# Kernel optimization log

Hardware: AMD Instinct MI355X
Metric: run time of the kernel (lower is better)

Reference implementation:

```python
import jax, jax.numpy as jnp
import numpy as np

D_MODEL = 1024
N_HEAD = 16
D_K = D_MODEL // N_HEAD
B, T = 4, 2048


def setup_inputs() -> dict:
    key = jax.random.key(0)
    ks = jax.random.split(key, 12)
    s = 1.0 / np.sqrt(D_MODEL)
    inp = {
        "q": jax.random.normal(ks[0], (B, T, D_MODEL), jnp.float32),
        "k": jax.random.normal(ks[1], (B, T, D_MODEL), jnp.float32),
        "v": jax.random.normal(ks[2], (B, T, D_MODEL), jnp.float32),
        # causal mask: True = allowed
        "mask": jnp.tril(jnp.ones((T, T), bool))[None, None, :, :],
        "w_q": jax.random.uniform(ks[3], (D_MODEL, D_MODEL), jnp.float32, -s, s),
        "b_q": jax.random.uniform(ks[4], (D_MODEL,), jnp.float32, -s, s),
        "w_k": jax.random.uniform(ks[5], (D_MODEL, D_MODEL), jnp.float32, -s, s),
        "b_k": jax.random.uniform(ks[6], (D_MODEL,), jnp.float32, -s, s),
        "w_v": jax.random.uniform(ks[7], (D_MODEL, D_MODEL), jnp.float32, -s, s),
        "b_v": jax.random.uniform(ks[8], (D_MODEL,), jnp.float32, -s, s),
        "w_o": jax.random.uniform(ks[9], (D_MODEL, D_MODEL), jnp.float32, -s, s),
        "b_o": jax.random.uniform(ks[10], (D_MODEL,), jnp.float32, -s, s),
    }
    return inp


def reference(q, k, v, mask, w_q, b_q, w_k, b_k, w_v, b_v, w_o, b_o):
    b, tq, d = q.shape
    tk = k.shape[1]
    # projections (torch Linear: x @ W^T + b)
    qh = (q @ w_q.T + b_q).reshape(b, tq, N_HEAD, D_K).transpose(0, 2, 1, 3)
    kh = (k @ w_k.T + b_k).reshape(b, tk, N_HEAD, D_K).transpose(0, 2, 1, 3)
    vh = (v @ w_v.T + b_v).reshape(b, tk, N_HEAD, D_K).transpose(0, 2, 1, 3)
    # scores: (b, h, tq, tk)
    scores = jnp.einsum("bhqd,bhkd->bhqk", qh, kh) / jnp.sqrt(jnp.float32(D_K))
    scores = jnp.where(mask, scores, jnp.finfo(scores.dtype).min)
    attn = jax.nn.softmax(scores, axis=-1)
    out = jnp.einsum("bhqk,bhkd->bhqd", attn, vh)
    out = out.transpose(0, 2, 1, 3).reshape(b, tq, d)
    return out @ w_o.T + b_o
```

## Files before the change

kernel.cpp:

```cpp
#include <hip/hip_runtime.h>

typedef unsigned short u16;
typedef __attribute__((ext_vector_type(8))) short bf16x8;
typedef __attribute__((ext_vector_type(4))) float f32x4;

#define D_MODEL 1024
#define T_SEQ   2048
#define NB      4
#define NH      16
#define DKH     64

__device__ __forceinline__ u16 f2bf(float x) {
  union { float f; unsigned u; } v; v.f = x;
  unsigned r = v.u + 0x7fffu + ((v.u >> 16) & 1u);
  return (u16)(r >> 16);
}
__device__ __forceinline__ unsigned pack2(float a, float b) {
  return (unsigned)f2bf(a) | ((unsigned)f2bf(b) << 16);
}

__device__ __forceinline__ void gload16(const void* g, void* l) {
  __builtin_amdgcn_global_load_lds(
      (const __attribute__((address_space(1))) unsigned*)g,
      (__attribute__((address_space(3))) unsigned*)l, 16, 0, 0);
}

__global__ void cast_w4(const float* __restrict__ s0, const float* __restrict__ s1,
                        const float* __restrict__ s2, const float* __restrict__ s3,
                        u16* __restrict__ o0, u16* __restrict__ o1,
                        u16* __restrict__ o2, u16* __restrict__ o3) {
  const int which = blockIdx.y;
  const float* s = which == 0 ? s0 : which == 1 ? s1 : which == 2 ? s2 : s3;
  u16* o = which == 0 ? o0 : which == 1 ? o1 : which == 2 ? o2 : o3;
  int i = ((int)blockIdx.x * 256 + (int)threadIdx.x) * 4;
  float4 v = *(const float4*)(s + i);
  uint2 u; u.x = pack2(v.x, v.y); u.y = pack2(v.z, v.w);
  *(uint2*)(o + i) = u;
}

__global__ void cast_x1(const float* __restrict__ s, u16* __restrict__ o) {
  size_t i = ((size_t)blockIdx.x * 256 + threadIdx.x) * 4;
  float4 v = *(const float4*)(s + i);
  uint2 u; u.x = pack2(v.x, v.y); u.y = pack2(v.z, v.w);
  *(uint2*)(o + i) = u;
}

template<int OUT_BF16>
__global__ __launch_bounds__(256) void gemm_nt(const u16* __restrict__ Ab,
                                               const u16* __restrict__ W,
                                               const float* __restrict__ bias,
                                               void* __restrict__ Cp,
                                               int M, int N, int K) {
  __shared__ __align__(16) u16 As[128 * 64];
  __shared__ __align__(16) u16 Bs[128 * 64];
  const int tid = threadIdx.x;
  const int w = tid >> 6, lane = tid & 63;
  const int wm = w & 1, wn = w >> 1;
  const int l15 = lane & 15, quad = lane >> 4;
  const int m0 = blockIdx.x * 128, n0 = blockIdx.y * 128;
  const int lrow = lane >> 3;
  const int lcol = ((lane & 7) ^ lrow) * 8;

  const u16* gA = Ab + (size_t)(m0 + w * 32 + lrow) * K + lcol;
  const u16* gB = W  + (size_t)(n0 + w * 32 + lrow) * K + lcol;
  u16* lA = As + w * 32 * 64;
  u16* lB = Bs + w * 32 * 64;

  f32x4 zero4 = {0.f, 0.f, 0.f, 0.f};
  f32x4 acc[4][4];
#pragma unroll
  for (int i = 0; i < 4; ++i)
#pragma unroll
    for (int j = 0; j < 4; ++j) acc[i][j] = zero4;

  for (int kb = 0; kb < K; kb += 64) {
    __syncthreads();
#pragma unroll
    for (int t = 0; t < 4; ++t) gload16(gA + kb + t * 8 * K, lA + t * 512);
#pragma unroll
    for (int t = 0; t < 4; ++t) gload16(gB + kb + t * 8 * K, lB + t * 512);
    __syncthreads();

#pragma unroll
    for (int ks = 0; ks < 2; ++ks) {
      const int sA = (((ks * 4 + quad) ^ (l15 & 7)) * 8);
      bf16x8 af[4], bfr[4];
#pragma unroll
      for (int i = 0; i < 4; ++i)
        af[i] = *(const bf16x8*)(As + (wm * 64 + i * 16 + l15) * 64 + sA);
#pragma unroll
      for (int i = 0; i < 4; ++i)
        bfr[i] = *(const bf16x8*)(Bs + (wn * 64 + i * 16 + l15) * 64 + sA);
#pragma unroll
      for (int mi = 0; mi < 4; ++mi)
#pragma unroll
        for (int ni = 0; ni < 4; ++ni)
          acc[mi][ni] = __builtin_amdgcn_mfma_f32_16x16x32_bf16(af[mi], bfr[ni], acc[mi][ni], 0, 0, 0);
    }
  }

#pragma unroll
  for (int ni = 0; ni < 4; ++ni) {
    int col = n0 + wn * 64 + ni * 16 + l15;
    float bv = bias[col];
#pragma unroll
    for (int mi = 0; mi < 4; ++mi) {
      int row = m0 + wm * 64 + mi * 16 + quad * 4;
#pragma unroll
      for (int r = 0; r < 4; ++r) {
        float vv = acc[mi][ni][r] + bv;
        if (OUT_BF16) ((u16*)Cp)[(size_t)(row + r) * N + col] = f2bf(vv);
        else          ((float*)Cp)[(size_t)(row + r) * N + col] = vv;
      }
    }
  }
}

__global__ __launch_bounds__(256) void attn_fwd(const u16* __restrict__ Xq,
                                                const u16* __restrict__ Xk,
                                                const u16* __restrict__ Xv,
                                                u16* __restrict__ O) {
  __shared__ __align__(16) u16 Vt[2][64 * 72];

  const int xp = blockIdx.x;
  const int h = blockIdx.y, b = blockIdx.z;
  const int tid = threadIdx.x;
  const int w = tid >> 6, lane = tid & 63;
  const int l15 = lane & 15, quad = lane >> 4;
  const size_t base = (size_t)b * T_SEQ * D_MODEL;
  const int hd = h * DKH;
  const int vkey = tid & 63, vdp = tid >> 6;
  const int skey = (vkey & 0x20) | ((vkey & 0xC) << 1) | ((vkey & 0x10) >> 2) | (vkey & 3);

  bf16x8 bones;
#pragma unroll
  for (int i = 0; i < 8; ++i) bones[i] = (short)0x3F80;

  f32x4 zero4 = {0.f, 0.f, 0.f, 0.f};
  int tcnt = 0;

  for (int ph = 0; ph < 2; ++ph) {
    const int qt = ph ? xp : 15 - xp;
    const int q0 = qt * 128;
    const int rowb0 = q0 + w * 32;

    bf16x8 bq[2][2];
#pragma unroll
    for (int mi = 0; mi < 2; ++mi)
#pragma unroll
      for (int ks = 0; ks < 2; ++ks)
        bq[mi][ks] = *(const bf16x8*)(Xq + base + (size_t)(rowb0 + mi * 16 + l15) * D_MODEL
                                      + hd + ks * 32 + quad * 8);

    f32x4 o[4][2], ol[2];
#pragma unroll
    for (int di = 0; di < 4; ++di)
#pragma unroll
      for (int mi = 0; mi < 2; ++mi) o[di][mi] = zero4;
#pragma unroll
    for (int mi = 0; mi < 2; ++mi) ol[mi] = zero4;
    float m_s[2] = {-1e30f, -1e30f};

    const int nkt = 2 * qt + 2;
    for (int kt = 0; kt < nkt; ++kt, ++tcnt) {
      const int k0 = kt * 64;
      const int buf = tcnt & 1;

      const u16* vp = Xv + base + (size_t)(k0 + vkey) * D_MODEL + hd + vdp * 16;
      uint4 va0 = *(const uint4*)vp;
      uint4 va1 = *(const uint4*)(vp + 8);

      bf16x8 ak[4][2];
#pragma unroll
      for (int ni = 0; ni < 4; ++ni) {
        const u16* kp = Xk + base + (size_t)(k0 + ni * 16 + l15) * D_MODEL + hd + quad * 8;
        ak[ni][0] = *(const bf16x8*)kp;
        ak[ni][1] = *(const bf16x8*)(kp + 32);
      }

      {
        union { uint4 u; u16 hh[8]; } u0, u1;
        u0.u = va0; u1.u = va1;
        u16* vtb = Vt[buf];
#pragma unroll
        for (int i = 0; i < 8; ++i) {
          vtb[(vdp * 16 + i) * 72 + skey] = u0.hh[i];
          vtb[(vdp * 16 + 8 + i) * 72 + skey] = u1.hh[i];
        }
      }

      f32x4 st[4][2];
#pragma unroll
      for (int ni = 0; ni < 4; ++ni)
#pragma unroll
        for (int mi = 0; mi < 2; ++mi) {
          f32x4 t = zero4;
          t = __builtin_amdgcn_mfma_f32_16x16x32_bf16(ak[ni][0], bq[mi][0], t, 0, 0, 0);
          t = __builtin_amdgcn_mfma_f32_16x16x32_bf16(ak[ni][1], bq[mi][1], t, 0, 0, 0);
          st[ni][mi] = t;
        }

      bf16x8 bp[2][2];
#pragma unroll
      for (int mi = 0; mi < 2; ++mi) {
        const int qa = rowb0 + mi * 16 + l15;
        if (k0 + 63 > rowb0 + mi * 16) {
#pragma unroll
          for (int ni = 0; ni < 4; ++ni)
#pragma unroll
            for (int r = 0; r < 4; ++r)
              if (k0 + ni * 16 + quad * 4 + r > qa) st[ni][mi][r] = -1e30f;
        }
        float mx = st[0][mi][0];
#pragma unroll
        for (int ni = 0; ni < 4; ++ni)
#pragma unroll
          for (int r = 0; r < 4; ++r) mx = fmaxf(mx, st[ni][mi][r]);
        mx = fmaxf(mx, __shfl_xor(mx, 16));
        mx = fmaxf(mx, __shfl_xor(mx, 32));
        float mnew = fmaxf(m_s[mi], mx * 0.125f);
        float a = __expf(m_s[mi] - mnew);
        m_s[mi] = mnew;
#pragma unroll
        for (int r = 0; r < 4; ++r) ol[mi][r] *= a;
#pragma unroll
        for (int di = 0; di < 4; ++di)
#pragma unroll
          for (int r = 0; r < 4; ++r) o[di][mi][r] *= a;

        float p[4][4];
#pragma unroll
        for (int ni = 0; ni < 4; ++ni)
#pragma unroll
          for (int r = 0; r < 4; ++r)
            p[ni][r] = __expf(st[ni][mi][r] * 0.125f - mnew);
#pragma unroll
        for (int js = 0; js < 2; ++js) {
          union { bf16x8 v; unsigned d[4]; } ub;
          ub.d[0] = pack2(p[2 * js][0], p[2 * js][1]);
          ub.d[1] = pack2(p[2 * js][2], p[2 * js][3]);
          ub.d[2] = pack2(p[2 * js + 1][0], p[2 * js + 1][1]);
          ub.d[3] = pack2(p[2 * js + 1][2], p[2 * js + 1][3]);
          bp[mi][js] = ub.v;
        }
      }

      __syncthreads();

#pragma unroll
      for (int js = 0; js < 2; ++js) {
        bf16x8 av[4];
#pragma unroll
        for (int di = 0; di < 4; ++di)
          av[di] = *(const bf16x8*)(Vt[buf] + (di * 16 + l15) * 72 + js * 32 + quad * 8);
#pragma unroll
        for (int di = 0; di < 4; ++di)
#pragma unroll
          for (int mi = 0; mi < 2; ++mi)
            o[di][mi] = __builtin_amdgcn_mfma_f32_16x16x32_bf16(av[di], bp[mi][js], o[di][mi], 0, 0, 0);
#pragma unroll
        for (int mi = 0; mi < 2; ++mi)
          ol[mi] = __builtin_amdgcn_mfma_f32_16x16x32_bf16(bones, bp[mi][js], ol[mi], 0, 0, 0);
      }
    }

#pragma unroll
    for (int mi = 0; mi < 2; ++mi) {
      float inv = 1.0f / ol[mi][0];
      const size_t qa = rowb0 + mi * 16 + l15;
#pragma unroll
      for (int di = 0; di < 4; ++di) {
        uint2 s2;
        s2.x = pack2(o[di][mi][0] * inv, o[di][mi][1] * inv);
        s2.y = pack2(o[di][mi][2] * inv, o[di][mi][3] * inv);
        *(uint2*)(O + base + qa * D_MODEL + hd + di * 16 + quad * 4) = s2;
      }
    }
  }
}

extern "C" void kernel_launch(void* const* d_in, const int* in_sizes, int n_in,
                              void* d_out, int out_size, void* d_ws, size_t ws_size,
                              hipStream_t stream) {
  const float* q   = (const float*)d_in[0];
  const float* k   = (const float*)d_in[1];
  const float* v   = (const float*)d_in[2];
  const float* w_q = (const float*)d_in[4];  const float* b_q = (const float*)d_in[5];
  const float* w_k = (const float*)d_in[6];  const float* b_k = (const float*)d_in[7];
  const float* w_v = (const float*)d_in[8];  const float* b_v = (const float*)d_in[9];
  const float* w_o = (const float*)d_in[10]; const float* b_o = (const float*)d_in[11];

  u16* ws = (u16*)d_ws;
  const size_t NTD = (size_t)NB * T_SEQ * D_MODEL;
  const size_t WSZ = (size_t)D_MODEL * D_MODEL;
  u16* wqb = ws;
  u16* wkb = wqb + WSZ;
  u16* wvb = wkb + WSZ;
  u16* wob = wvb + WSZ;
  u16* Xq  = wob + WSZ;
  u16* Xk  = Xq + NTD;
  u16* Xv  = Xk + NTD;
  u16* Cb  = Xv + NTD;

  cast_w4<<<dim3(WSZ / 1024, 4), 256, 0, stream>>>(w_q, w_k, w_v, w_o, wqb, wkb, wvb, wob);

  dim3 g(64, 8, 1);
  cast_x1<<<NTD / 1024, 256, 0, stream>>>(q, Cb);
  gemm_nt<1><<<g, 256, 0, stream>>>(Cb, wqb, b_q, Xq, 8192, 1024, 1024);
  cast_x1<<<NTD / 1024, 256, 0, stream>>>(k, Cb);
  gemm_nt<1><<<g, 256, 0, stream>>>(Cb, wkb, b_k, Xk, 8192, 1024, 1024);
  cast_x1<<<NTD / 1024, 256, 0, stream>>>(v, Cb);
  gemm_nt<1><<<g, 256, 0, stream>>>(Cb, wvb, b_v, Xv, 8192, 1024, 1024);

  attn_fwd<<<dim3(8, NH, NB), 256, 0, stream>>>(Xq, Xk, Xv, Cb);

  gemm_nt<0><<<g, 256, 0, stream>>>(Cb, wob, b_o, d_out, 8192, 1024, 1024);
}
```

Before: 371.1 us.

## Fuse input cast into batched QKV GEMM and retile attention with prefetch

Replaces the separate fp32-to-bf16 cast kernels and three projection GEMMs with one batched QKV GEMM that reads fp32 activations and converts them in registers before storing to padded LDS. This drops the intermediate bf16 activation round-trip and several launches. The attention kernel moves from 128-row to 64-row query tiles with twice as many blocks, register-prefetches the next K/V tile, and uses exp2 with a folded scale. The cost is more register pressure from the prefetch and A loads that no longer use async global-to-LDS copies.

```diff
diff --git a/kernel.cpp b/kernel.cpp
--- a/kernel.cpp
+++ b/kernel.cpp
@@ -17,6 +17,13 @@
 }
 __device__ __forceinline__ unsigned pack2(float a, float b) {
   return (unsigned)f2bf(a) | ((unsigned)f2bf(b) << 16);
+}
+__device__ __forceinline__ float fexp2(float x) {
+#if __has_builtin(__builtin_amdgcn_exp2f)
+  return __builtin_amdgcn_exp2f(x);
+#else
+  return __expf(x * 0.6931471805599453f);
+#endif
 }
 
 __device__ __forceinline__ void gload16(const void* g, void* l) {
@@ -38,19 +45,95 @@
   *(uint2*)(o + i) = u;
 }
 
-__global__ void cast_x1(const float* __restrict__ s, u16* __restrict__ o) {
-  size_t i = ((size_t)blockIdx.x * 256 + threadIdx.x) * 4;
-  float4 v = *(const float4*)(s + i);
-  uint2 u; u.x = pack2(v.x, v.y); u.y = pack2(v.z, v.w);
-  *(uint2*)(o + i) = u;
-}
-
-template<int OUT_BF16>
-__global__ __launch_bounds__(256) void gemm_nt(const u16* __restrict__ Ab,
-                                               const u16* __restrict__ W,
-                                               const float* __restrict__ bias,
-                                               void* __restrict__ Cp,
-                                               int M, int N, int K) {
+__global__ __launch_bounds__(256) void gemm_qkv(
+    const float* __restrict__ qin, const float* __restrict__ kin, const float* __restrict__ vin,
+    const u16* __restrict__ wq, const u16* __restrict__ wk, const u16* __restrict__ wv,
+    const float* __restrict__ bqp, const float* __restrict__ bkp, const float* __restrict__ bvp,
+    u16* __restrict__ Xq, u16* __restrict__ Xk, u16* __restrict__ Xv) {
+  const int z = blockIdx.z;
+  const float* A = z == 0 ? qin : z == 1 ? kin : vin;
+  const u16* W = z == 0 ? wq : z == 1 ? wk : wv;
+  const float* bias = z == 0 ? bqp : z == 1 ? bkp : bvp;
+  u16* C = z == 0 ? Xq : z == 1 ? Xk : Xv;
+  const int K = 1024, N = 1024;
+
+  __shared__ __align__(16) u16 As[128 * 72];
+  __shared__ __align__(16) u16 Bs[128 * 64];
+  const int tid = threadIdx.x;
+  const int w = tid >> 6, lane = tid & 63;
+  const int wm = w & 1, wn = w >> 1;
+  const int l15 = lane & 15, quad = lane >> 4;
+  const int m0 = blockIdx.x * 128, n0 = blockIdx.y * 128;
+  const int srow = tid >> 3;
+  const int scol = (tid & 7) * 8;
+  const int lrow = lane >> 3;
+  const int lcol = ((lane & 7) ^ lrow) * 8;
+
+  const u16* gB = W + (size_t)(n0 + w * 32 + lrow) * K + lcol;
+  u16* lB = Bs + w * 32 * 64;
+
+  f32x4 zero4 = {0.f, 0.f, 0.f, 0.f};
+  f32x4 acc[4][4];
+#pragma unroll
+  for (int i = 0; i < 4; ++i)
+#pragma unroll
+    for (int j = 0; j < 4; ++j) acc[i][j] = zero4;
+
+  for (int kb = 0; kb < K; kb += 64) {
+    uint4 ra[4];
+#pragma unroll
+    for (int r = 0; r < 4; ++r) {
+      const float* p = A + (size_t)(m0 + r * 32 + srow) * K + kb + scol;
+      float4 x = *(const float4*)p;
+      float4 y = *(const float4*)(p + 4);
+      ra[r].x = pack2(x.x, x.y); ra[r].y = pack2(x.z, x.w);
+      ra[r].z = pack2(y.x, y.y); ra[r].w = pack2(y.z, y.w);
+    }
+    __syncthreads();
+#pragma unroll
+    for (int t = 0; t < 4; ++t) gload16(gB + kb + t * 8 * K, lB + t * 512);
+#pragma unroll
+    for (int r = 0; r < 4; ++r)
+      *(uint4*)(As + (r * 32 + srow) * 72 + scol) = ra[r];
+    __syncthreads();
+
+#pragma unroll
+    for (int ks = 0; ks < 2; ++ks) {
+      const int sB = (((ks * 4 + quad) ^ (l15 & 7)) * 8);
+      bf16x8 af[4], bfr[4];
+#pragma unroll
+      for (int i = 0; i < 4; ++i)
+        af[i] = *(const bf16x8*)(As + (wm * 64 + i * 16 + l15) * 72 + ks * 32 + quad * 8);
+#pragma unroll
+      for (int i = 0; i < 4; ++i)
+        bfr[i] = *(const bf16x8*)(Bs + (wn * 64 + i * 16 + l15) * 64 + sB);
+#pragma unroll
+      for (int mi = 0; mi < 4; ++mi)
+#pragma unroll
+        for (int ni = 0; ni < 4; ++ni)
+          acc[mi][ni] = __builtin_amdgcn_mfma_f32_16x16x32_bf16(af[mi], bfr[ni], acc[mi][ni], 0, 0, 0);
+    }
+  }
+
+#pragma unroll
+  for (int ni = 0; ni < 4; ++ni) {
+    int col = n0 + wn * 64 + ni * 16 + l15;
+    float bv = bias[col];
+#pragma unroll
+    for (int mi = 0; mi < 4; ++mi) {
+      int row = m0 + wm * 64 + mi * 16 + quad * 4;
+#pragma unroll
+      for (int r = 0; r < 4; ++r)
+        C[(size_t)(row + r) * N + col] = f2bf(acc[mi][ni][r] + bv);
+    }
+  }
+}
+
+__global__ __launch_bounds__(256) void gemm_nt_f32out(const u16* __restrict__ Ab,
+                                                      const u16* __restrict__ W,
+                                                      const float* __restrict__ bias,
+                                                      float* __restrict__ Cp,
+                                                      int M, int N, int K) {
   __shared__ __align__(16) u16 As[128 * 64];
   __shared__ __align__(16) u16 Bs[128 * 64];
   const int tid = threadIdx.x;
@@ -107,11 +190,8 @@
     for (int mi = 0; mi < 4; ++mi) {
       int row = m0 + wm * 64 + mi * 16 + quad * 4;
 #pragma unroll
-      for (int r = 0; r < 4; ++r) {
-        float vv = acc[mi][ni][r] + bv;
-        if (OUT_BF16) ((u16*)Cp)[(size_t)(row + r) * N + col] = f2bf(vv);
-        else          ((float*)Cp)[(size_t)(row + r) * N + col] = vv;
-      }
+      for (int r = 0; r < 4; ++r)
+        Cp[(size_t)(row + r) * N + col] = acc[mi][ni][r] + bv;
     }
   }
 }
@@ -136,47 +216,47 @@
 #pragma unroll
   for (int i = 0; i < 8; ++i) bones[i] = (short)0x3F80;
 
+  const float cs = 0.18033688f;
   f32x4 zero4 = {0.f, 0.f, 0.f, 0.f};
   int tcnt = 0;
 
   for (int ph = 0; ph < 2; ++ph) {
-    const int qt = ph ? xp : 15 - xp;
-    const int q0 = qt * 128;
-    const int rowb0 = q0 + w * 32;
-
-    bf16x8 bq[2][2];
-#pragma unroll
-    for (int mi = 0; mi < 2; ++mi)
-#pragma unroll
-      for (int ks = 0; ks < 2; ++ks)
-        bq[mi][ks] = *(const bf16x8*)(Xq + base + (size_t)(rowb0 + mi * 16 + l15) * D_MODEL
-                                      + hd + ks * 32 + quad * 8);
-
-    f32x4 o[4][2], ol[2];
-#pragma unroll
-    for (int di = 0; di < 4; ++di)
-#pragma unroll
-      for (int mi = 0; mi < 2; ++mi) o[di][mi] = zero4;
-#pragma unroll
-    for (int mi = 0; mi < 2; ++mi) ol[mi] = zero4;
-    float m_s[2] = {-1e30f, -1e30f};
-
-    const int nkt = 2 * qt + 2;
+    const int qt = ph ? xp : 31 - xp;
+    const int q0 = qt * 64;
+    const int rowb = q0 + w * 16;
+    const int qa = rowb + l15;
+
+    bf16x8 bq[2];
+#pragma unroll
+    for (int ks = 0; ks < 2; ++ks)
+      bq[ks] = *(const bf16x8*)(Xq + base + (size_t)(rowb + l15) * D_MODEL
+                                + hd + ks * 32 + quad * 8);
+
+    f32x4 o[4], ol;
+#pragma unroll
+    for (int di = 0; di < 4; ++di) o[di] = zero4;
+    ol = zero4;
+    float m2 = -1e30f;
+
+    const int nkt = qt + 1;
+
+    uint4 va0, va1;
+    bf16x8 ak[4][2];
+    {
+      const u16* vp = Xv + base + (size_t)vkey * D_MODEL + hd + vdp * 16;
+      va0 = *(const uint4*)vp;
+      va1 = *(const uint4*)(vp + 8);
+#pragma unroll
+      for (int ni = 0; ni < 4; ++ni) {
+        const u16* kp = Xk + base + (size_t)(ni * 16 + l15) * D_MODEL + hd + quad * 8;
+        ak[ni][0] = *(const bf16x8*)kp;
+        ak[ni][1] = *(const bf16x8*)(kp + 32);
+      }
+    }
+
     for (int kt = 0; kt < nkt; ++kt, ++tcnt) {
       const int k0 = kt * 64;
       const int buf = tcnt & 1;
-
-      const u16* vp = Xv + base + (size_t)(k0 + vkey) * D_MODEL + hd + vdp * 16;
-      uint4 va0 = *(const uint4*)vp;
-      uint4 va1 = *(const uint4*)(vp + 8);
-
-      bf16x8 ak[4][2];
-#pragma unroll
-      for (int ni = 0; ni < 4; ++ni) {
-        const u16* kp = Xk + base + (size_t)(k0 + ni * 16 + l15) * D_MODEL + hd + quad * 8;
-        ak[ni][0] = *(const bf16x8*)kp;
-        ak[ni][1] = *(const bf16x8*)(kp + 32);
-      }
 
       {
         union { uint4 u; u16 hh[8]; } u0, u1;
@@ -189,60 +269,71 @@
         }
       }
 
-      f32x4 st[4][2];
+      const bool pf = (kt + 1 < nkt);
+      uint4 nva0, nva1;
+      bf16x8 nak[4][2];
+      if (pf) {
+        const int nk0 = k0 + 64;
+        const u16* vp = Xv + base + (size_t)(nk0 + vkey) * D_MODEL + hd + vdp * 16;
+        nva0 = *(const uint4*)vp;
+        nva1 = *(const uint4*)(vp + 8);
+#pragma unroll
+        for (int ni = 0; ni < 4; ++ni) {
+          const u16* kp = Xk + base + (size_t)(nk0 + ni * 16 + l15) * D_MODEL + hd + quad * 8;
+          nak[ni][0] = *(const bf16x8*)kp;
+          nak[ni][1] = *(const bf16x8*)(kp + 32);
+        }
+      }
+
+      f32x4 st[4];
+#pragma unroll
+      for (int ni = 0; ni < 4; ++ni) {
+        f32x4 t = zero4;
+        t = __builtin_amdgcn_mfma_f32_16x16x32_bf16(ak[ni][0], bq[0], t, 0, 0, 0);
+        t = __builtin_amdgcn_mfma_f32_16x16x32_bf16(ak[ni][1], bq[1], t, 0, 0, 0);
+        st[ni] = t;
+      }
+
+      if (k0 + 63 > rowb) {
+#pragma unroll
+        for (int ni = 0; ni < 4; ++ni)
+#pragma unroll
+          for (int r = 0; r < 4; ++r)
+            if (k0 + ni * 16 + quad * 4 + r > qa) st[ni][r] = -1e30f;
+      }
+
+      float mx = st[0][0];
 #pragma unroll
       for (int ni = 0; ni < 4; ++ni)
 #pragma unroll
-        for (int mi = 0; mi < 2; ++mi) {
-          f32x4 t = zero4;
-          t = __builtin_amdgcn_mfma_f32_16x16x32_bf16(ak[ni][0], bq[mi][0], t, 0, 0, 0);
-          t = __builtin_amdgcn_mfma_f32_16x16x32_bf16(ak[ni][1], bq[mi][1], t, 0, 0, 0);
-          st[ni][mi] = t;
-        }
-
-      bf16x8 bp[2][2];
-#pragma unroll
-      for (int mi = 0; mi < 2; ++mi) {
-        const int qa = rowb0 + mi * 16 + l15;
-        if (k0 + 63 > rowb0 + mi * 16) {
-#pragma unroll
-          for (int ni = 0; ni < 4; ++ni)
-#pragma unroll
-            for (int r = 0; r < 4; ++r)
-              if (k0 + ni * 16 + quad * 4 + r > qa) st[ni][mi][r] = -1e30f;
-        }
-        float mx = st[0][mi][0];
-#pragma unroll
-        for (int ni = 0; ni < 4; ++ni)
-#pragma unroll
-          for (int r = 0; r < 4; ++r) mx = fmaxf(mx, st[ni][mi][r]);
-        mx = fmaxf(mx, __shfl_xor(mx, 16));
-        mx = fmaxf(mx, __shfl_xor(mx, 32));
-        float mnew = fmaxf(m_s[mi], mx * 0.125f);
-        float a = __expf(m_s[mi] - mnew);
-        m_s[mi] = mnew;
-#pragma unroll
-        for (int r = 0; r < 4; ++r) ol[mi][r] *= a;
-#pragma unroll
-        for (int di = 0; di < 4; ++di)
-#pragma unroll
-          for (int r = 0; r < 4; ++r) o[di][mi][r] *= a;
-
-        float p[4][4];
-#pragma unroll
-        for (int ni = 0; ni < 4; ++ni)
-#pragma unroll
-          for (int r = 0; r < 4; ++r)
-            p[ni][r] = __expf(st[ni][mi][r] * 0.125f - mnew);
-#pragma unroll
-        for (int js = 0; js < 2; ++js) {
-          union { bf16x8 v; unsigned d[4]; } ub;
-          ub.d[0] = pack2(p[2 * js][0], p[2 * js][1]);
-          ub.d[1] = pack2(p[2 * js][2], p[2 * js][3]);
-          ub.d[2] = pack2(p[2 * js + 1][0], p[2 * js + 1][1]);
-          ub.d[3] = pack2(p[2 * js + 1][2], p[2 * js + 1][3]);
-          bp[mi][js] = ub.v;
-        }
+        for (int r = 0; r < 4; ++r) mx = fmaxf(mx, st[ni][r]);
+      mx = fmaxf(mx, __shfl_xor(mx, 16));
+      mx = fmaxf(mx, __shfl_xor(mx, 32));
+      const float m2new = fmaxf(m2, mx * cs);
+      const float a = fexp2(m2 - m2new);
+      m2 = m2new;
+      ol[0] *= a;
+#pragma unroll
+      for (int di = 0; di < 4; ++di)
+#pragma unroll
+        for (int r = 0; r < 4; ++r) o[di][r] *= a;
+
+      float p[4][4];
+#pragma unroll
+      for (int ni = 0; ni < 4; ++ni)
+#pragma unroll
+        for (int r = 0; r < 4; ++r)
+          p[ni][r] = fexp2(fmaf(st[ni][r], cs, -m2new));
+
+      bf16x8 bp[2];
+#pragma unroll
+      for (int js = 0; js < 2; ++js) {
+        union { bf16x8 v; unsigned d[4]; } ub;
+        ub.d[0] = pack2(p[2 * js][0], p[2 * js][1]);
+        ub.d[1] = pack2(p[2 * js][2], p[2 * js][3]);
+        ub.d[2] = pack2(p[2 * js + 1][0], p[2 * js + 1][1]);
+        ub.d[3] = pack2(p[2 * js + 1][2], p[2 * js + 1][3]);
+        bp[js] = ub.v;
       }
 
       __syncthreads();
@@ -255,26 +346,27 @@
           av[di] = *(const bf16x8*)(Vt[buf] + (di * 16 + l15) * 72 + js * 32 + quad * 8);
 #pragma unroll
         for (int di = 0; di < 4; ++di)
-#pragma unroll
-          for (int mi = 0; mi < 2; ++mi)
-            o[di][mi] = __builtin_amdgcn_mfma_f32_16x16x32_bf16(av[di], bp[mi][js], o[di][mi], 0, 0, 0);
-#pragma unroll
-        for (int mi = 0; mi < 2; ++mi)
-          ol[mi] = __builtin_amdgcn_mfma_f32_16x16x32_bf16(bones, bp[mi][js], ol[mi], 0, 0, 0);
-      }
-    }
-
-#pragma unroll
-    for (int mi = 0; mi < 2; ++mi) {
-      float inv = 1.0f / ol[mi][0];
-      const size_t qa = rowb0 + mi * 16 + l15;
-#pragma unroll
-      for (int di = 0; di < 4; ++di) {
-        uint2 s2;
-        s2.x = pack2(o[di][mi][0] * inv, o[di][mi][1] * inv);
-        s2.y = pack2(o[di][mi][2] * inv, o[di][mi][3] * inv);
-        *(uint2*)(O + base + qa * D_MODEL + hd + di * 16 + quad * 4) = s2;
-      }
+          o[di] = __builtin_amdgcn_mfma_f32_16x16x32_bf16(av[di], bp[js], o[di], 0, 0, 0);
+        ol = __builtin_amdgcn_mfma_f32_16x16x32_bf16(bones, bp[js], ol, 0, 0, 0);
+      }
+
+      if (pf) {
+        va0 = nva0; va1 = nva1;
+#pragma unroll
+        for (int ni = 0; ni < 4; ++ni) {
+          ak[ni][0] = nak[ni][0];
+          ak[ni][1] = nak[ni][1];
+        }
+      }
+    }
+
+    const float inv = 1.0f / ol[0];
+#pragma unroll
+    for (int di = 0; di < 4; ++di) {
+      uint2 s2;
+      s2.x = pack2(o[di][0] * inv, o[di][1] * inv);
+      s2.y = pack2(o[di][2] * inv, o[di][3] * inv);
+      *(uint2*)(O + base + (size_t)qa * D_MODEL + hd + di * 16 + quad * 4) = s2;
     }
   }
 }
@@ -300,19 +392,15 @@
   u16* Xq  = wob + WSZ;
   u16* Xk  = Xq + NTD;
   u16* Xv  = Xk + NTD;
-  u16* Cb  = Xv + NTD;
+  u16* Ob  = Xv + NTD;
 
   cast_w4<<<dim3(WSZ / 1024, 4), 256, 0, stream>>>(w_q, w_k, w_v, w_o, wqb, wkb, wvb, wob);
 
-  dim3 g(64, 8, 1);
-  cast_x1<<<NTD / 1024, 256, 0, stream>>>(q, Cb);
-  gemm_nt<1><<<g, 256, 0, stream>>>(Cb, wqb, b_q, Xq, 8192, 1024, 1024);
-  cast_x1<<<NTD / 1024, 256, 0, stream>>>(k, Cb);
-  gemm_nt<1><<<g, 256, 0, stream>>>(Cb, wkb, b_k, Xk, 8192, 1024, 1024);
-  cast_x1<<<NTD / 1024, 256, 0, stream>>>(v, Cb);
-  gemm_nt<1><<<g, 256, 0, stream>>>(Cb, wvb, b_v, Xv, 8192, 1024, 1024);
-
-  attn_fwd<<<dim3(8, NH, NB), 256, 0, stream>>>(Xq, Xk, Xv, Cb);
-
-  gemm_nt<0><<<g, 256, 0, stream>>>(Cb, wob, b_o, d_out, 8192, 1024, 1024);
-}
+  gemm_qkv<<<dim3(64, 8, 3), 256, 0, stream>>>(q, k, v, wqb, wkb, wvb,
+                                               b_q, b_k, b_v, Xq, Xk, Xv);
+
+  attn_fwd<<<dim3(16, NH, NB), 256, 0, stream>>>(Xq, Xk, Xv, Ob);
+
+  gemm_nt_f32out<<<dim3(64, 8), 256, 0, stream>>>(Ob, wob, b_o, (float*)d_out,
+                                                  8192, 1024, 1024);
+}
```

Result: slower. 429.1 us (+15.6%).
